# Kernel optimization log

Hardware: AMD Instinct MI355X
Metric: run time of the kernel (lower is better)

The kernel has to match this reference:

```python
import math
import jax, jax.numpy as jnp
import numpy as np

B, T, D = 4, 1024, 1024
H = 16
HD = D // H       # head_dim
DE = 64           # d_event
NT = 8            # n_event_types
NR = 64           # n_rules
NH = 4            # n_hits
NA = 2            # n_alternatives
SQ = math.sqrt(HD)


def setup_inputs() -> dict:
    key = jax.random.key(0)
    ks = jax.random.split(key, 16)
    s = 0.02
    f = jnp.float32
    return {
        "x": jax.random.normal(ks[0], (B, T, D), f),
        "W_node": jax.random.normal(ks[1], (D, D), f) * s,
        "W_value": jax.random.normal(ks[2], (D, D), f) * s,
        "W_out": jax.random.normal(ks[3], (D, D), f) * s,
        "arity_w": jax.random.normal(ks[4], (H, HD), f) * s,   # arity=3 -> one extra axis weight
        "W_event": jax.random.normal(ks[5], (D, DE), f) * s,
        "W_type": jax.random.normal(ks[6], (D, NT), f) * s,
        "patterns": jax.random.normal(ks[7], (NR, DE), f) * s,
        "W_actions": jax.random.normal(ks[8], (NA, D, D), f) * s,
        "W_alt": jax.random.normal(ks[9], (DE, NA), f) * s,
        "log_temp": jnp.zeros((), f),
        "Wg1": jax.random.normal(ks[10], (2 * D + 1, D), f) * s,
        "bg1": jnp.zeros((D,), f),
        "Wg2": jax.random.normal(ks[11], (D, 1), f) * s,
        "bg2": jnp.zeros((1,), f),
    }


def reference(x, W_node, W_value, W_out, arity_w, W_event, W_type, patterns,
              W_actions, W_alt, log_temp, Wg1, bg1, Wg2, bg2):
    # --- IsotropicAttention (arity=3, eval mode so dropout is identity) ---
    nodes = (x @ W_node).reshape(B, T, H, HD).transpose(0, 2, 1, 3)    # (B,H,T,HD)
    values = (x @ W_value).reshape(B, T, H, HD).transpose(0, 2, 1, 3)  # (B,H,T,HD)
    scores = jnp.einsum('bhtd,bhsd->bhts', nodes, nodes)
    scores = (scores + scores.transpose(0, 1, 3, 2)) * (0.5 / SQ)      # symmetrize + scale
    ax = jnp.einsum('bhtd,hd->bht', nodes, arity_w)                    # ternary axis score
    mod = jax.nn.sigmoid((ax[:, :, :, None] + ax[:, :, None, :]) / SQ)
    scores = scores * mod
    attn = jax.nn.softmax(scores, axis=-1)
    attn_out = jnp.einsum('bhts,bhsd->bthd', attn, values).reshape(B, T, D) @ W_out
    x1 = x + attn_out
    # --- EventGenerator ---
    events = x1 @ W_event                                              # (B,T,DE)
    event_types = jax.nn.softmax(x1 @ W_type, axis=-1)                 # (B,T,NT)
    # --- RuleBank: soft top-k hit activation ---
    en = events / jnp.maximum(jnp.linalg.norm(events, axis=-1, keepdims=True), 1e-12)
    pn = patterns / jnp.maximum(jnp.linalg.norm(patterns, axis=-1, keepdims=True), 1e-12)
    sim = en @ pn.T                                                    # (B,T,NR)
    topk_vals, topk_idx = jax.lax.top_k(sim, NH)
    temp = jnp.clip(jnp.exp(log_temp), 0.01, 10.0)
    hit_w = jax.nn.softmax(topk_vals / temp, axis=-1)                  # (B,T,NH)
    hit_patterns = patterns[topk_idx]                                  # (B,T,NH,DE)
    weighted_pattern = jnp.einsum('btkd,btk->btd', hit_patterns, hit_w)
    alt_w = jax.nn.softmax((weighted_pattern @ W_alt) / temp, axis=-1) # (B,T,NA)
    acted = jnp.einsum('btd,ade->btae', x1, W_actions)                 # (B,T,NA,D)
    actions_out = jnp.einsum('btae,bta->bte', acted, alt_w)
    hit_strength = jnp.max(topk_vals, axis=-1, keepdims=True)
    actions_out = actions_out * jax.nn.sigmoid(hit_strength)
    # --- TransactionGate: soft commit/rollback ---
    entropy = -jnp.sum(event_types * jnp.log(event_types + 1e-10), axis=-1, keepdims=True)
    entropy_norm = entropy / math.log(NT)
    gin = jnp.concatenate([x1, actions_out, entropy_norm], axis=-1)    # (B,T,2D+1)
    g = jax.nn.sigmoid(jax.nn.silu(gin @ Wg1 + bg1) @ Wg2 + bg2)       # (B,T,1)
    return x1 + g * actions_out
```

## Files before the change

### kernel.cpp

```cpp
#include <hip/hip_runtime.h>
#include <hip/hip_bf16.h>
#include <math.h>

#define B_  4
#define T_  1024
#define D_  1024
#define H_  16
#define HD_ 64
#define DE_ 64
#define NT_ 8
#define NR_ 64
#define NH_ 4

typedef __attribute__((ext_vector_type(8))) short short8;
typedef __attribute__((ext_vector_type(4))) short short4v;
typedef __attribute__((ext_vector_type(2))) unsigned uint2v;
typedef __attribute__((ext_vector_type(4))) float f4;

__device__ __forceinline__ short f2bf(float f) {
    unsigned x = __float_as_uint(f);
    unsigned r = (x + 0x7fffu + ((x >> 16) & 1u)) >> 16;
    return (short)r;
}
__device__ __forceinline__ float bf2f(short s) {
    return __uint_as_float(((unsigned)(unsigned short)s) << 16);
}

__device__ __forceinline__ int swz64(int row, int slot) {
    return row * 64 + ((slot ^ (row & 7)) << 3);
}

__global__ __launch_bounds__(256) void castx_k(
    const float* __restrict__ x, short* __restrict__ xb)
{
    size_t i = ((size_t)blockIdx.x * 256 + threadIdx.x) * 8;
    float4 v0 = *(const float4*)&x[i];
    float4 v1 = *(const float4*)&x[i + 4];
    short8 o;
    o[0] = f2bf(v0.x); o[1] = f2bf(v0.y); o[2] = f2bf(v0.z); o[3] = f2bf(v0.w);
    o[4] = f2bf(v1.x); o[5] = f2bf(v1.y); o[6] = f2bf(v1.z); o[7] = f2bf(v1.w);
    *(short8*)&xb[i] = o;
}

struct TJ { const float* src; short* dst; int K, N, rs, ro, base; };
struct TJobs { TJ j[7]; };

__global__ __launch_bounds__(256) void tcast_all(TJobs jb)
{
    int bid = blockIdx.x;
    int ji = 0;
#pragma unroll
    for (int i = 1; i < 7; i++) if (bid >= jb.j[i].base) ji = i;
    const float* src = jb.j[ji].src;
    short* dst = jb.j[ji].dst;
    const int K = jb.j[ji].K, N = jb.j[ji].N;
    const int rs = jb.j[ji].rs, ro = jb.j[ji].ro;
    int rel = bid - jb.j[ji].base;
    int tiles_n = N >> 6;
    int k0 = (rel / tiles_n) * 64, n0 = (rel % tiles_n) * 64;

    __shared__ float tile[64][65];
    const int tid = threadIdx.x;
    const int r = tid >> 4, c = (tid & 15) * 4;
#pragma unroll
    for (int rep = 0; rep < 4; rep++) {
        int rr = rep * 16 + r;
        float4 v = *(const float4*)&src[(size_t)(k0 + rr) * N + n0 + c];
        tile[rr][c] = v.x; tile[rr][c + 1] = v.y; tile[rr][c + 2] = v.z; tile[rr][c + 3] = v.w;
    }
    __syncthreads();
#pragma unroll
    for (int rep = 0; rep < 4; rep++) {
        int n = rep * 16 + r;
        short4v p;
        p[0] = f2bf(tile[c + 0][n]);
        p[1] = f2bf(tile[c + 1][n]);
        p[2] = f2bf(tile[c + 2][n]);
        p[3] = f2bf(tile[c + 3][n]);
        *(short4v*)&dst[(size_t)((n0 + n) * rs + ro) * K + k0 + c] = p;
    }
}

__global__ __launch_bounds__(256) void ttype_k(
    const float* __restrict__ Wt, short* __restrict__ BTe)
{
    int idx = blockIdx.x * 256 + threadIdx.x;
    int n = idx >> 10, k = idx & 1023;
    BTe[(size_t)(64 + n) * 1024 + k] = f2bf(Wt[k * 8 + n]);
}

template<int AM>
__global__ __launch_bounds__(256) void gemm8(
    const short* __restrict__ A1, const short* __restrict__ A2, int Ks,
    const short* __restrict__ BT,
    float* __restrict__ C, short* __restrict__ Cb1, short* __restrict__ Cb2,
    int M, int N, int K, int epi,
    const float* __restrict__ resid, const float* __restrict__ ent,
    const float* __restrict__ w1e, const float* __restrict__ bias,
    const float* __restrict__ altw, const float* __restrict__ hitsig)
{
    constexpr int BM = AM * 32;
    constexpr int AR = (AM == 4) ? 2 : 4;
    constexpr int ANV = 64 / AR / 8;
    __shared__ short As[BM * 72];
    __shared__ short Bs[64 * 72];
    const int tid = threadIdx.x, wave = tid >> 6, lane = tid & 63;
    const int lrow = lane & 15, lq = lane >> 4;
    int bid = blockIdx.x;
    int tiles_m = M / BM;
    int mpx = tiles_m >> 3;
    int xcd = bid & 7, idx = bid >> 3;
    int mt = xcd * mpx + (idx % mpx);
    int nt = idx / mpx;
    const int m0 = mt * BM, n0 = nt * 64;
    const int wm = (wave >> 1) * (AM * 16), wn = (wave & 1) * 32;
    const int K2 = K - Ks;
    const int arow = tid / AR, ash = (tid % AR) * (64 / AR);
    const int brow = tid >> 2, bsh = (tid & 3) * 16;

    short8 va[ANV], vb[2];
    auto loadA = [&](int k0) {
        int ka = k0 + ash;
        const short* ap = (ka < Ks)
            ? A1 + (size_t)(m0 + arow) * Ks + ka
            : A2 + (size_t)(m0 + arow) * K2 + (ka - Ks);
#pragma unroll
        for (int u = 0; u < ANV; u++) va[u] = *(const short8*)(ap + u * 8);
    };
    auto loadB = [&](int k0) {
        const short* bp = BT + (size_t)(n0 + brow) * K + k0 + bsh;
#pragma unroll
        for (int u = 0; u < 2; u++) vb[u] = *(const short8*)(bp + u * 8);
    };

    loadA(0); loadB(0);
    f4 acc[AM][2] = {};

    for (int k0 = 0; k0 < K; k0 += 64) {
        __syncthreads();
#pragma unroll
        for (int u = 0; u < ANV; u++)
            *(short8*)&As[arow * 72 + ash + u * 8] = va[u];
#pragma unroll
        for (int u = 0; u < 2; u++)
            *(short8*)&Bs[brow * 72 + bsh + u * 8] = vb[u];
        __syncthreads();
        if (k0 + 64 < K) { loadA(k0 + 64); loadB(k0 + 64); }
        __builtin_amdgcn_sched_barrier(0);
#pragma unroll
        for (int kh = 0; kh < 2; kh++) {
            short8 af[AM], bfv[2];
#pragma unroll
            for (int i = 0; i < AM; i++)
                af[i] = *(short8*)&As[(wm + i * 16 + lrow) * 72 + kh * 32 + lq * 8];
#pragma unroll
            for (int j = 0; j < 2; j++)
                bfv[j] = *(short8*)&Bs[(wn + j * 16 + lrow) * 72 + kh * 32 + lq * 8];
#pragma unroll
            for (int i = 0; i < AM; i++)
#pragma unroll
                for (int j = 0; j < 2; j++)
                    acc[i][j] = __builtin_amdgcn_mfma_f32_16x16x32_bf16(
                        af[i], bfv[j], acc[i][j], 0, 0, 0);
        }
    }

#pragma unroll
    for (int i = 0; i < AM; i++) {
#pragma unroll
        for (int r = 0; r < 4; r++) {
            int row = m0 + wm + i * 16 + lq * 4 + r;
            float w0 = 0.f, w1 = 0.f, hs = 0.f;
            if (epi == 5) { w0 = altw[row * 2]; w1 = altw[row * 2 + 1]; hs = hitsig[row]; }
#pragma unroll
            for (int j = 0; j < 2; j++) {
                int col = n0 + wn + j * 16 + lrow;
                float v = acc[i][j][r];
                if (epi == 0) {
                    C[(size_t)row * N + col] = v;
                } else if (epi == 1) {
                    v += resid[(size_t)row * N + col];
                    C[(size_t)row * N + col] = v;
                    Cb1[(size_t)row * N + col] = f2bf(v);
                } else if (epi == 2) {
                    if (col < 1024) Cb1[(size_t)row * 1024 + col] = f2bf(v);
                    else            Cb2[(size_t)row * 1024 + col - 1024] = f2bf(v);
                } else if (epi == 3) {
                    v += ent[row] * w1e[col] + bias[col];
                    float sv = v * __builtin_amdgcn_rcpf(1.f + __expf(-v));
                    Cb1[(size_t)row * N + col] = f2bf(sv);
                } else {
                    float other = __shfl_xor(v, 1);
                    if ((lane & 1) == 0) {
                        float cv = (w0 * v + w1 * other) * hs;
                        Cb1[(size_t)row * 1024 + (col >> 1)] = f2bf(cv);
                    }
                }
            }
        }
    }
}

__global__ __launch_bounds__(256) void vtrans_k(
    const short* __restrict__ vb, short* __restrict__ vtg)
{
    const int b = blockIdx.z, h = blockIdx.y, t0 = blockIdx.x * 64;
    const int tid = threadIdx.x;
    __shared__ short tile[64 * 72];
    const int row = tid >> 2, c = (tid & 3) * 16;
    const short* p = vb + (size_t)(b * T_ + t0 + row) * D_ + h * 64 + c;
    *(short8*)&tile[row * 72 + c + 0] = *(const short8*)(p + 0);
    *(short8*)&tile[row * 72 + c + 8] = *(const short8*)(p + 8);
    __syncthreads();
    short8 o0, o1;
#pragma unroll
    for (int i = 0; i < 8; i++) o0[i] = tile[(c + i) * 72 + row];
#pragma unroll
    for (int i = 0; i < 8; i++) o1[i] = tile[(c + 8 + i) * 72 + row];
    short* q = vtg + (size_t)((b * H_ + h) * 64 + row) * T_ + t0 + c;
    *(short8*)(q + 0) = o0;
    *(short8*)(q + 8) = o1;
}

__global__ __launch_bounds__(256) void ax_k(
    const short* __restrict__ nodes_bf, const float* __restrict__ arity_w,
    float* __restrict__ ax)
{
    int idx = blockIdx.x * 256 + threadIdx.x;
    int t = idx & (T_ - 1);
    int h = (idx >> 10) & (H_ - 1);
    int b = idx >> 14;
    const short* np_ = nodes_bf + (((size_t)b * T_ + t) * H_ + h) * HD_;
    float s = 0.f;
#pragma unroll
    for (int d = 0; d < HD_; d += 8) {
        short8 n8 = *(const short8*)&np_[d];
#pragma unroll
        for (int q = 0; q < 8; q++) s += bf2f(n8[q]) * arity_w[h * HD_ + d + q];
    }
    ax[idx] = s;
}

__global__ __launch_bounds__(256) void attn9_k(
    const short* __restrict__ nodes_bf, const short* __restrict__ vtg,
    const float* __restrict__ ax, short* __restrict__ attnp)
{
    const int b = blockIdx.z, h = blockIdx.y, t0 = blockIdx.x * 64;
    const int tid = threadIdx.x;
    const int wave = tid >> 6, lane = tid & 63;
    const int lrow = lane & 15, lq = lane >> 4;
    const int wm = wave * 16;
    const int row = tid >> 2, c4 = tid & 3;

    __shared__ short Ns[2][64 * 64];
    __shared__ short Vt[2][64 * 64];
    __shared__ short Pm[64 * 64];

    const short* qp = nodes_bf + (size_t)(b * T_ + t0 + wm + lrow) * D_ + h * 64;
    const short8 bt0 = *(const short8*)(qp + lq * 8);
    const short8 bt1 = *(const short8*)(qp + 32 + lq * 8);
    const float at8 = ax[(size_t)(b * H_ + h) * T_ + t0 + wm + lrow] * 0.125f;

    const short* np0 = nodes_bf + (size_t)(b * T_ + row) * D_ + h * 64 + c4 * 16;
    const short* vp0 = vtg + (size_t)((b * H_ + h) * 64 + row) * T_ + c4 * 16;
    const float* axp_ = ax + (size_t)(b * H_ + h) * T_;

    short8 vn0, vn1, vv0, vv1;
    f4 axv[4];
    auto preload = [&](int s0) {
        const short* np = np0 + (size_t)s0 * D_;
        const short* vp = vp0 + s0;
        vn0 = *(const short8*)(np + 0);
        vn1 = *(const short8*)(np + 8);
        vv0 = *(const short8*)(vp + 0);
        vv1 = *(const short8*)(vp + 8);
#pragma unroll
        for (int j = 0; j < 4; j++)
            axv[j] = *(const f4*)&axp_[s0 + j * 16 + lq * 4];
    };

    preload(0);

    float l_reg = 0.f;
    f4 O[4] = {};
    f4 axc[4];

    for (int t = 0; t < T_ / 64; t++) {
        const int cur = t & 1;
        *(short8*)&Ns[cur][swz64(row, 2 * c4 + 0)] = vn0;
        *(short8*)&Ns[cur][swz64(row, 2 * c4 + 1)] = vn1;
        *(short8*)&Vt[cur][swz64(row, 2 * c4 + 0)] = vv0;
        *(short8*)&Vt[cur][swz64(row, 2 * c4 + 1)] = vv1;
#pragma unroll
        for (int j = 0; j < 4; j++) axc[j] = axv[j];
        __syncthreads();
        if (t + 1 < T_ / 64) preload((t + 1) * 64);
        __builtin_amdgcn_sched_barrier(0);

        float psum = 0.f;
#pragma unroll
        for (int j = 0; j < 4; j++) {
            short8 a0 = *(short8*)&Ns[cur][swz64(j * 16 + lrow, lq)];
            short8 a1 = *(short8*)&Ns[cur][swz64(j * 16 + lrow, 4 + lq)];
            f4 s = {0.f, 0.f, 0.f, 0.f};
            __builtin_amdgcn_s_setprio(1);
            s = __builtin_amdgcn_mfma_f32_16x16x32_bf16(a0, bt0, s, 0, 0, 0);
            s = __builtin_amdgcn_mfma_f32_16x16x32_bf16(a1, bt1, s, 0, 0, 0);
            __builtin_amdgcn_s_setprio(0);
            float p0, p1, p2, p3;
            {
                float z, zz, t1, mK;
                z = fmaf(axc[j][0], 0.125f, at8); zz = z * z;
                t1 = fmaf(zz, -0.0037570183f, 0.04508422f);
                mK = fmaf(z, t1, 0.09016844f);
                p0 = __builtin_amdgcn_exp2f(s[0] * mK);
                z = fmaf(axc[j][1], 0.125f, at8); zz = z * z;
                t1 = fmaf(zz, -0.0037570183f, 0.04508422f);
                mK = fmaf(z, t1, 0.09016844f);
                p1 = __builtin_amdgcn_exp2f(s[1] * mK);
                z = fmaf(axc[j][2], 0.125f, at8); zz = z * z;
                t1 = fmaf(zz, -0.0037570183f, 0.04508422f);
                mK = fmaf(z, t1, 0.09016844f);
                p2 = __builtin_amdgcn_exp2f(s[2] * mK);
                z = fmaf(axc[j][3], 0.125f, at8); zz = z * z;
                t1 = fmaf(zz, -0.0037570183f, 0.04508422f);
                mK = fmaf(z, t1, 0.09016844f);
                p3 = __builtin_amdgcn_exp2f(s[3] * mK);
            }
            psum += (p0 + p1) + (p2 + p3);
            unsigned u0, u1;
            asm("v_cvt_pk_bf16_f32 %0, %1, %2" : "=v"(u0) : "v"(p0), "v"(p1));
            asm("v_cvt_pk_bf16_f32 %0, %1, %2" : "=v"(u1) : "v"(p2), "v"(p3));
            uint2v uu; uu[0] = u0; uu[1] = u1;
            *(uint2v*)&Pm[swz64(wm + lrow, 2 * j + (lq >> 1)) + (lq & 1) * 4] = uu;
        }
        l_reg += psum;

        short8 pa0 = *(short8*)&Pm[swz64(wm + lrow, lq)];
        short8 pa1 = *(short8*)&Pm[swz64(wm + lrow, 4 + lq)];
        __builtin_amdgcn_s_setprio(1);
#pragma unroll
        for (int dj = 0; dj < 4; dj++) {
            short8 v0 = *(short8*)&Vt[cur][swz64(dj * 16 + lrow, lq)];
            short8 v1 = *(short8*)&Vt[cur][swz64(dj * 16 + lrow, 4 + lq)];
            O[dj] = __builtin_amdgcn_mfma_f32_16x16x32_bf16(pa0, v0, O[dj], 0, 0, 0);
            O[dj] = __builtin_amdgcn_mfma_f32_16x16x32_bf16(pa1, v1, O[dj], 0, 0, 0);
        }
        __builtin_amdgcn_s_setprio(0);
    }

    l_reg += __shfl_xor(l_reg, 16);
    l_reg += __shfl_xor(l_reg, 32);

    float linv[4];
#pragma unroll
    for (int r = 0; r < 4; r++)
        linv[r] = __builtin_amdgcn_rcpf(__shfl(l_reg, lq * 4 + r));
#pragma unroll
    for (int dj = 0; dj < 4; dj++)
#pragma unroll
        for (int r = 0; r < 4; r++)
            attnp[(size_t)(b * T_ + t0 + wm + lq * 4 + r) * D_ + h * 64 + dj * 16 + lrow] =
                f2bf(O[dj][r] * linv[r]);
}

__global__ __launch_bounds__(64) void pnorm_k(
    const float* __restrict__ patterns, float* __restrict__ pn)
{
    int r = blockIdx.x, lane = threadIdx.x;
    float v = patterns[r * 64 + lane];
    float ss = v * v;
    for (int off = 1; off < 64; off <<= 1) ss += __shfl_xor(ss, off);
    pn[r * 64 + lane] = v / fmaxf(sqrtf(ss), 1e-12f);
}

__global__ __launch_bounds__(256) void token2_k(
    const float* __restrict__ evlg, const float* __restrict__ pn,
    const float* __restrict__ patterns, const float* __restrict__ W_alt,
    const float* __restrict__ log_temp,
    float* __restrict__ entn, float* __restrict__ altw, float* __restrict__ hitsig)
{
    const int tid = threadIdx.x, wave = tid >> 6, lane = tid & 63;
    __shared__ float pn_sh[64 * 68];
    __shared__ float pat_sh[64 * 68];
    __shared__ float en_sh[4][68];
    {
        int row = tid >> 2, c = (tid & 3) * 16;
#pragma unroll
        for (int u = 0; u < 4; u++) {
            *(float4*)&pn_sh[row * 68 + c + u * 4]  = *(const float4*)&pn[row * 64 + c + u * 4];
            *(float4*)&pat_sh[row * 68 + c + u * 4] = *(const float4*)&patterns[row * 64 + c + u * 4];
        }
    }
    float temp = expf(log_temp[0]);
    temp = fminf(fmaxf(temp, 0.01f), 10.f);
    const float tinv = 1.f / temp;
    __syncthreads();

#pragma unroll
    for (int rep = 0; rep < 2; rep++) {
        const int m = blockIdx.x * 8 + wave * 2 + rep;
        float ev = evlg[(size_t)m * 128 + lane];
        float ss = ev * ev;
        for (int off = 1; off < 64; off <<= 1) ss += __shfl_xor(ss, off);
        float en = ev * __builtin_amdgcn_rcpf(fmaxf(sqrtf(ss), 1e-12f));
        en_sh[wave][lane] = en;
        float entv;
        {
            float lgt = evlg[(size_t)m * 128 + 64 + (lane & 7)];
            float mx = lgt;
            for (int off = 1; off < 8; off <<= 1) mx = fmaxf(mx, __shfl_xor(mx, off));
            float p = __expf(lgt - mx);
            float sum = p;
            for (int off = 1; off < 8; off <<= 1) sum += __shfl_xor(sum, off);
            float pi = p / sum;
            float term = -pi * __logf(pi + 1e-10f);
            float e = term;
            for (int off = 1; off < 8; off <<= 1) e += __shfl_xor(e, off);
            entv = e * 0.4808983f;
        }
        float sim = 0.f;
#pragma unroll
        for (int u = 0; u < 16; u++) {
            float4 e4 = *(float4*)&en_sh[wave][u * 4];
            float4 p4 = *(float4*)&pn_sh[lane * 68 + u * 4];
            sim += e4.x * p4.x + e4.y * p4.y + e4.z * p4.z + e4.w * p4.w;
        }
        float v = sim;
        float tv[NH_]; int tix[NH_];
#pragma unroll
        for (int kk = 0; kk < NH_; kk++) {
            float mv = v; int mi = lane;
            if (v == -1e30f) mi = 127;
            for (int off = 1; off < 64; off <<= 1) {
                float ov = __shfl_xor(mv, off);
                int   oi = __shfl_xor(mi, off);
                if (ov > mv || (ov == mv && oi < mi)) { mv = ov; mi = oi; }
            }
            tv[kk] = mv; tix[kk] = mi;
            if (lane == mi) v = -1e30f;
        }
        float hmx = tv[0];
        float hw[NH_], hsum = 0.f;
#pragma unroll
        for (int kk = 0; kk < NH_; kk++) { hw[kk] = __expf((tv[kk] - hmx) * tinv); hsum += hw[kk]; }
        float hsr = __builtin_amdgcn_rcpf(hsum);
        float wp = 0.f;
#pragma unroll
        for (int kk = 0; kk < NH_; kk++) wp += hw[kk] * hsr * pat_sh[tix[kk] * 68 + lane];
        float a0 = wp * W_alt[lane * 2 + 0];
        float a1 = wp * W_alt[lane * 2 + 1];
        for (int off = 1; off < 64; off <<= 1) {
            a0 += __shfl_xor(a0, off);
            a1 += __shfl_xor(a1, off);
        }
        a0 *= tinv; a1 *= tinv;
        float amx = fmaxf(a0, a1);
        float e0 = __expf(a0 - amx), e1 = __expf(a1 - amx);
        if (lane == 0) {
            float zr = __builtin_amdgcn_rcpf(e0 + e1);
            altw[m * 2 + 0] = e0 * zr;
            altw[m * 2 + 1] = e1 * zr;
            hitsig[m] = __builtin_amdgcn_rcpf(1.f + __expf(-tv[0]));
            entn[m] = entv;
        }
    }
}

__global__ __launch_bounds__(256) void gate_k(
    const short* __restrict__ h1_bf, const float* __restrict__ Wg2,
    const float* __restrict__ bg2, const float* __restrict__ x1,
    const short* __restrict__ actions_bf, float* __restrict__ out)
{
    const int m = blockIdx.x, tid = threadIdx.x;
    float part = 0.f;
    for (int d = tid; d < D_; d += 256)
        part += bf2f(h1_bf[(size_t)m * D_ + d]) * Wg2[d];
    __shared__ float red[256];
    red[tid] = part;
    __syncthreads();
    for (int w = 128; w > 0; w >>= 1) {
        if (tid < w) red[tid] += red[tid + w];
        __syncthreads();
    }
    float g = 1.f / (1.f + expf(-(red[0] + bg2[0])));
    for (int d = tid; d < D_; d += 256) {
        size_t i = (size_t)m * D_ + d;
        out[i] = x1[i] + g * bf2f(actions_bf[i]);
    }
}

extern "C" void kernel_launch(void* const* d_in, const int* in_sizes, int n_in,
                              void* d_out, int out_size, void* d_ws, size_t ws_size,
                              hipStream_t stream)
{
    const float* x        = (const float*)d_in[0];
    const float* W_node   = (const float*)d_in[1];
    const float* W_value  = (const float*)d_in[2];
    const float* W_out    = (const float*)d_in[3];
    const float* arity_w  = (const float*)d_in[4];
    const float* W_event  = (const float*)d_in[5];
    const float* W_type   = (const float*)d_in[6];
    const float* patterns = (const float*)d_in[7];
    const float* W_act    = (const float*)d_in[8];
    const float* W_alt    = (const float*)d_in[9];
    const float* log_temp = (const float*)d_in[10];
    const float* Wg1      = (const float*)d_in[11];
    const float* bg1      = (const float*)d_in[12];
    const float* Wg2      = (const float*)d_in[13];
    const float* bg2      = (const float*)d_in[14];
    float* out = (float*)d_out;

    const int M = B_ * T_;
    float* x1     = (float*)d_ws;
    float* evlg   = x1 + 4194304;
    float* axp    = evlg + 524288;
    float* pn     = axp + 65536;
    float* entn   = pn + 4096;
    float* altw   = entn + 4096;
    float* hitsig = altw + 8192;
    short* big       = (short*)(hitsig + 4096);
    short* xbf       = big;
    short* nodes_bf  = big + 1 * 4194304;
    short* values_bf = big + 2 * 4194304;
    short* vtg       = big + 3 * 4194304;
    short* x1_bf     = big + 4 * 4194304;
    short* wts       = big + 5 * 4194304;
    short* WnvT  = wts;
    short* WoT   = wts + 2 * 1048576;
    short* WaT   = wts + 3 * 1048576;
    short* Wg1T  = wts + 5 * 1048576;
    short* BTe   = wts + 7 * 1048576;
    short* actions_bf = vtg;
    short* h1_bf      = xbf;

    dim3 blk(256);
    dim3 g_bh(T_ / 64, H_, B_);

    castx_k<<<2048, blk, 0, stream>>>(x, xbf);
    pnorm_k<<<NR_, 64, 0, stream>>>(patterns, pn);
    TJobs jb;
    jb.j[0] = {W_node,            WnvT,           1024, 1024, 1, 0,    0};
    jb.j[1] = {W_value,           WnvT + 1048576, 1024, 1024, 1, 0,  256};
    jb.j[2] = {W_out,             WoT,            1024, 1024, 1, 0,  512};
    jb.j[3] = {W_act,             WaT,            1024, 1024, 2, 0,  768};
    jb.j[4] = {W_act + 1048576,   WaT,            1024, 1024, 2, 1, 1024};
    jb.j[5] = {Wg1,               Wg1T,           2048, 1024, 1, 0, 1280};
    jb.j[6] = {W_event,           BTe,            1024,   64, 1, 0, 1792};
    tcast_all<<<1808, blk, 0, stream>>>(jb);
    ttype_k<<<32, blk, 0, stream>>>(W_type, BTe);

    gemm8<4><<<1024, blk, 0, stream>>>(xbf, xbf, D_, WnvT,
        nullptr, nodes_bf, values_bf, M, 2048, D_, 2,
        nullptr, nullptr, nullptr, nullptr, nullptr, nullptr);
    ax_k<<<256, blk, 0, stream>>>(nodes_bf, arity_w, axp);
    vtrans_k<<<g_bh, blk, 0, stream>>>(values_bf, vtg);
    attn9_k<<<g_bh, blk, 0, stream>>>(nodes_bf, vtg, axp, xbf);
    gemm8<2><<<1024, blk, 0, stream>>>(xbf, xbf, D_, WoT,
        x1, x1_bf, nullptr, M, D_, D_, 1,
        x, nullptr, nullptr, nullptr, nullptr, nullptr);
    gemm8<2><<<128, blk, 0, stream>>>(x1_bf, x1_bf, D_, BTe,
        evlg, nullptr, nullptr, M, 128, D_, 0,
        nullptr, nullptr, nullptr, nullptr, nullptr, nullptr);
    token2_k<<<M / 8, blk, 0, stream>>>(evlg, pn, patterns, W_alt, log_temp,
                                        entn, altw, hitsig);
    gemm8<4><<<1024, blk, 0, stream>>>(x1_bf, x1_bf, D_, WaT,
        nullptr, actions_bf, nullptr, M, 2048, D_, 5,
        nullptr, nullptr, nullptr, nullptr, altw, hitsig);
    gemm8<2><<<1024, blk, 0, stream>>>(x1_bf, actions_bf, D_, Wg1T,
        nullptr, h1_bf, nullptr, M, D_, 2048, 3,
        nullptr, entn, Wg1 + (size_t)2048 * D_, bg1, nullptr, nullptr);
    gate_k<<<M, blk, 0, stream>>>(h1_bf, Wg2, bg2, x1, actions_bf, out);
}
```

Baseline: 321.4 us.

## Fuse gate dot product into GEMM epilogue and merge small prep kernels

```diff
diff --git a/kernel.cpp b/kernel.cpp
--- a/kernel.cpp
+++ b/kernel.cpp
@@ -30,63 +30,73 @@
     return row * 64 + ((slot ^ (row & 7)) << 3);
 }
 
-__global__ __launch_bounds__(256) void castx_k(
-    const float* __restrict__ x, short* __restrict__ xb)
-{
-    size_t i = ((size_t)blockIdx.x * 256 + threadIdx.x) * 8;
-    float4 v0 = *(const float4*)&x[i];
-    float4 v1 = *(const float4*)&x[i + 4];
-    short8 o;
-    o[0] = f2bf(v0.x); o[1] = f2bf(v0.y); o[2] = f2bf(v0.z); o[3] = f2bf(v0.w);
-    o[4] = f2bf(v1.x); o[5] = f2bf(v1.y); o[6] = f2bf(v1.z); o[7] = f2bf(v1.w);
-    *(short8*)&xb[i] = o;
-}
-
 struct TJ { const float* src; short* dst; int K, N, rs, ro, base; };
 struct TJobs { TJ j[7]; };
 
-__global__ __launch_bounds__(256) void tcast_all(TJobs jb)
-{
-    int bid = blockIdx.x;
-    int ji = 0;
-#pragma unroll
-    for (int i = 1; i < 7; i++) if (bid >= jb.j[i].base) ji = i;
-    const float* src = jb.j[ji].src;
-    short* dst = jb.j[ji].dst;
-    const int K = jb.j[ji].K, N = jb.j[ji].N;
-    const int rs = jb.j[ji].rs, ro = jb.j[ji].ro;
-    int rel = bid - jb.j[ji].base;
-    int tiles_n = N >> 6;
-    int k0 = (rel / tiles_n) * 64, n0 = (rel % tiles_n) * 64;
-
+__global__ __launch_bounds__(256) void prep_k(
+    const float* __restrict__ x, short* __restrict__ xb, TJobs jb,
+    const float* __restrict__ Wt, short* __restrict__ BTe,
+    const float* __restrict__ patterns, float* __restrict__ pn)
+{
+    const int bid = blockIdx.x;
+    const int tid = threadIdx.x;
     __shared__ float tile[64][65];
-    const int tid = threadIdx.x;
-    const int r = tid >> 4, c = (tid & 15) * 4;
-#pragma unroll
-    for (int rep = 0; rep < 4; rep++) {
-        int rr = rep * 16 + r;
-        float4 v = *(const float4*)&src[(size_t)(k0 + rr) * N + n0 + c];
-        tile[rr][c] = v.x; tile[rr][c + 1] = v.y; tile[rr][c + 2] = v.z; tile[rr][c + 3] = v.w;
-    }
-    __syncthreads();
-#pragma unroll
-    for (int rep = 0; rep < 4; rep++) {
-        int n = rep * 16 + r;
-        short4v p;
-        p[0] = f2bf(tile[c + 0][n]);
-        p[1] = f2bf(tile[c + 1][n]);
-        p[2] = f2bf(tile[c + 2][n]);
-        p[3] = f2bf(tile[c + 3][n]);
-        *(short4v*)&dst[(size_t)((n0 + n) * rs + ro) * K + k0 + c] = p;
-    }
-}
-
-__global__ __launch_bounds__(256) void ttype_k(
-    const float* __restrict__ Wt, short* __restrict__ BTe)
-{
-    int idx = blockIdx.x * 256 + threadIdx.x;
-    int n = idx >> 10, k = idx & 1023;
-    BTe[(size_t)(64 + n) * 1024 + k] = f2bf(Wt[k * 8 + n]);
+
+    if (bid < 2048) {
+        size_t i = ((size_t)bid * 256 + tid) * 8;
+        float4 v0 = *(const float4*)&x[i];
+        float4 v1 = *(const float4*)&x[i + 4];
+        short8 o;
+        o[0] = f2bf(v0.x); o[1] = f2bf(v0.y); o[2] = f2bf(v0.z); o[3] = f2bf(v0.w);
+        o[4] = f2bf(v1.x); o[5] = f2bf(v1.y); o[6] = f2bf(v1.z); o[7] = f2bf(v1.w);
+        *(short8*)&xb[i] = o;
+        return;
+    }
+    if (bid < 3856) {
+        int ji = 0;
+#pragma unroll
+        for (int i = 1; i < 7; i++) if (bid >= jb.j[i].base) ji = i;
+        const float* src = jb.j[ji].src;
+        short* dst = jb.j[ji].dst;
+        const int K = jb.j[ji].K, N = jb.j[ji].N;
+        const int rs = jb.j[ji].rs, ro = jb.j[ji].ro;
+        int rel = bid - jb.j[ji].base;
+        int tiles_n = N >> 6;
+        int k0 = (rel / tiles_n) * 64, n0 = (rel % tiles_n) * 64;
+        const int r = tid >> 4, c = (tid & 15) * 4;
+#pragma unroll
+        for (int rep = 0; rep < 4; rep++) {
+            int rr = rep * 16 + r;
+            float4 v = *(const float4*)&src[(size_t)(k0 + rr) * N + n0 + c];
+            tile[rr][c] = v.x; tile[rr][c + 1] = v.y; tile[rr][c + 2] = v.z; tile[rr][c + 3] = v.w;
+        }
+        __syncthreads();
+#pragma unroll
+        for (int rep = 0; rep < 4; rep++) {
+            int n = rep * 16 + r;
+            short4v p;
+            p[0] = f2bf(tile[c + 0][n]);
+            p[1] = f2bf(tile[c + 1][n]);
+            p[2] = f2bf(tile[c + 2][n]);
+            p[3] = f2bf(tile[c + 3][n]);
+            *(short4v*)&dst[(size_t)((n0 + n) * rs + ro) * K + k0 + c] = p;
+        }
+        return;
+    }
+    if (bid < 3888) {
+        int idx = (bid - 3856) * 256 + tid;
+        int n = idx >> 10, k = idx & 1023;
+        BTe[(size_t)(64 + n) * 1024 + k] = f2bf(Wt[k * 8 + n]);
+        return;
+    }
+    {
+        int r = (bid - 3888) * 4 + (tid >> 6);
+        int lane = tid & 63;
+        float v = patterns[r * 64 + lane];
+        float ss = v * v;
+        for (int off = 1; off < 64; off <<= 1) ss += __shfl_xor(ss, off);
+        pn[r * 64 + lane] = v / fmaxf(sqrtf(ss), 1e-12f);
+    }
 }
 
 template<int AM>
@@ -165,6 +175,30 @@
         }
     }
 
+    if (epi == 3) {
+#pragma unroll
+        for (int i = 0; i < AM; i++) {
+#pragma unroll
+            for (int r = 0; r < 4; r++) {
+                int row = m0 + wm + i * 16 + lq * 4 + r;
+                float gp = 0.f;
+#pragma unroll
+                for (int j = 0; j < 2; j++) {
+                    int col = n0 + wn + j * 16 + lrow;
+                    float v = acc[i][j][r] + ent[row] * w1e[col] + bias[col];
+                    float sv = v * __builtin_amdgcn_rcpf(1.f + __expf(-v));
+                    gp += sv * altw[col];
+                }
+                gp += __shfl_xor(gp, 1);
+                gp += __shfl_xor(gp, 2);
+                gp += __shfl_xor(gp, 4);
+                gp += __shfl_xor(gp, 8);
+                if (lrow == 0) atomicAdd(&C[row], gp);
+            }
+        }
+        return;
+    }
+
 #pragma unroll
     for (int i = 0; i < AM; i++) {
 #pragma unroll
@@ -185,10 +219,6 @@
                 } else if (epi == 2) {
                     if (col < 1024) Cb1[(size_t)row * 1024 + col] = f2bf(v);
                     else            Cb2[(size_t)row * 1024 + col - 1024] = f2bf(v);
-                } else if (epi == 3) {
-                    v += ent[row] * w1e[col] + bias[col];
-                    float sv = v * __builtin_amdgcn_rcpf(1.f + __expf(-v));
-                    Cb1[(size_t)row * N + col] = f2bf(sv);
                 } else {
                     float other = __shfl_xor(v, 1);
                     if ((lane & 1) == 0) {
@@ -201,44 +231,47 @@
     }
 }
 
-__global__ __launch_bounds__(256) void vtrans_k(
-    const short* __restrict__ vb, short* __restrict__ vtg)
-{
-    const int b = blockIdx.z, h = blockIdx.y, t0 = blockIdx.x * 64;
+__global__ __launch_bounds__(256) void vx_k(
+    const short* __restrict__ vb, short* __restrict__ vtg,
+    const short* __restrict__ nodes_bf, const float* __restrict__ arity_w,
+    float* __restrict__ ax)
+{
+    const int bid = blockIdx.x;
     const int tid = threadIdx.x;
     __shared__ short tile[64 * 72];
-    const int row = tid >> 2, c = (tid & 3) * 16;
-    const short* p = vb + (size_t)(b * T_ + t0 + row) * D_ + h * 64 + c;
-    *(short8*)&tile[row * 72 + c + 0] = *(const short8*)(p + 0);
-    *(short8*)&tile[row * 72 + c + 8] = *(const short8*)(p + 8);
-    __syncthreads();
-    short8 o0, o1;
-#pragma unroll
-    for (int i = 0; i < 8; i++) o0[i] = tile[(c + i) * 72 + row];
-#pragma unroll
-    for (int i = 0; i < 8; i++) o1[i] = tile[(c + 8 + i) * 72 + row];
-    short* q = vtg + (size_t)((b * H_ + h) * 64 + row) * T_ + t0 + c;
-    *(short8*)(q + 0) = o0;
-    *(short8*)(q + 8) = o1;
-}
-
-__global__ __launch_bounds__(256) void ax_k(
-    const short* __restrict__ nodes_bf, const float* __restrict__ arity_w,
-    float* __restrict__ ax)
-{
-    int idx = blockIdx.x * 256 + threadIdx.x;
-    int t = idx & (T_ - 1);
-    int h = (idx >> 10) & (H_ - 1);
-    int b = idx >> 14;
-    const short* np_ = nodes_bf + (((size_t)b * T_ + t) * H_ + h) * HD_;
-    float s = 0.f;
-#pragma unroll
-    for (int d = 0; d < HD_; d += 8) {
-        short8 n8 = *(const short8*)&np_[d];
-#pragma unroll
-        for (int q = 0; q < 8; q++) s += bf2f(n8[q]) * arity_w[h * HD_ + d + q];
-    }
-    ax[idx] = s;
+
+    if (bid < 1024) {
+        const int b = bid >> 8, h = (bid >> 4) & 15, t0 = (bid & 15) * 64;
+        const int row = tid >> 2, c = (tid & 3) * 16;
+        const short* p = vb + (size_t)(b * T_ + t0 + row) * D_ + h * 64 + c;
+        *(short8*)&tile[row * 72 + c + 0] = *(const short8*)(p + 0);
+        *(short8*)&tile[row * 72 + c + 8] = *(const short8*)(p + 8);
+        __syncthreads();
+        short8 o0, o1;
+#pragma unroll
+        for (int i = 0; i < 8; i++) o0[i] = tile[(c + i) * 72 + row];
+#pragma unroll
+        for (int i = 0; i < 8; i++) o1[i] = tile[(c + 8 + i) * 72 + row];
+        short* q = vtg + (size_t)((b * H_ + h) * 64 + row) * T_ + t0 + c;
+        *(short8*)(q + 0) = o0;
+        *(short8*)(q + 8) = o1;
+        return;
+    }
+    {
+        int idx = (bid - 1024) * 256 + tid;
+        int t = idx & (T_ - 1);
+        int h = (idx >> 10) & (H_ - 1);
+        int b = idx >> 14;
+        const short* np_ = nodes_bf + (((size_t)b * T_ + t) * H_ + h) * HD_;
+        float s = 0.f;
+#pragma unroll
+        for (int d = 0; d < HD_; d += 8) {
+            short8 n8 = *(const short8*)&np_[d];
+#pragma unroll
+            for (int q = 0; q < 8; q++) s += bf2f(n8[q]) * arity_w[h * HD_ + d + q];
+        }
+        ax[idx] = s;
+    }
 }
 
 __global__ __launch_bounds__(256) void attn9_k(
@@ -364,21 +397,12 @@
                 f2bf(O[dj][r] * linv[r]);
 }
 
-__global__ __launch_bounds__(64) void pnorm_k(
-    const float* __restrict__ patterns, float* __restrict__ pn)
-{
-    int r = blockIdx.x, lane = threadIdx.x;
-    float v = patterns[r * 64 + lane];
-    float ss = v * v;
-    for (int off = 1; off < 64; off <<= 1) ss += __shfl_xor(ss, off);
-    pn[r * 64 + lane] = v / fmaxf(sqrtf(ss), 1e-12f);
-}
-
 __global__ __launch_bounds__(256) void token2_k(
     const float* __restrict__ evlg, const float* __restrict__ pn,
     const float* __restrict__ patterns, const float* __restrict__ W_alt,
     const float* __restrict__ log_temp,
-    float* __restrict__ entn, float* __restrict__ altw, float* __restrict__ hitsig)
+    float* __restrict__ entn, float* __restrict__ altw, float* __restrict__ hitsig,
+    float* __restrict__ gsum)
 {
     const int tid = threadIdx.x, wave = tid >> 6, lane = tid & 63;
     __shared__ float pn_sh[64 * 68];
@@ -463,31 +487,27 @@
             altw[m * 2 + 1] = e1 * zr;
             hitsig[m] = __builtin_amdgcn_rcpf(1.f + __expf(-tv[0]));
             entn[m] = entv;
-        }
-    }
-}
-
-__global__ __launch_bounds__(256) void gate_k(
-    const short* __restrict__ h1_bf, const float* __restrict__ Wg2,
-    const float* __restrict__ bg2, const float* __restrict__ x1,
-    const short* __restrict__ actions_bf, float* __restrict__ out)
+            gsum[m] = 0.f;
+        }
+    }
+}
+
+__global__ __launch_bounds__(256) void gate2_k(
+    const float* __restrict__ gsum, const float* __restrict__ bg2,
+    const float* __restrict__ x1, const short* __restrict__ actions_bf,
+    float* __restrict__ out)
 {
     const int m = blockIdx.x, tid = threadIdx.x;
-    float part = 0.f;
-    for (int d = tid; d < D_; d += 256)
-        part += bf2f(h1_bf[(size_t)m * D_ + d]) * Wg2[d];
-    __shared__ float red[256];
-    red[tid] = part;
-    __syncthreads();
-    for (int w = 128; w > 0; w >>= 1) {
-        if (tid < w) red[tid] += red[tid + w];
-        __syncthreads();
-    }
-    float g = 1.f / (1.f + expf(-(red[0] + bg2[0])));
-    for (int d = tid; d < D_; d += 256) {
-        size_t i = (size_t)m * D_ + d;
-        out[i] = x1[i] + g * bf2f(actions_bf[i]);
-    }
+    float g = 1.f / (1.f + __expf(-(gsum[m] + bg2[0])));
+    size_t i = (size_t)m * D_ + tid * 4;
+    float4 xv = *(const float4*)&x1[i];
+    short4v av = *(const short4v*)&actions_bf[i];
+    float4 o;
+    o.x = xv.x + g * bf2f(av[0]);
+    o.y = xv.y + g * bf2f(av[1]);
+    o.z = xv.z + g * bf2f(av[2]);
+    o.w = xv.w + g * bf2f(av[3]);
+    *(float4*)&out[i] = o;
 }
 
 extern "C" void kernel_launch(void* const* d_in, const int* in_sizes, int n_in,
@@ -519,6 +539,7 @@
     float* entn   = pn + 4096;
     float* altw   = entn + 4096;
     float* hitsig = altw + 8192;
+    float* gsum   = axp;
     short* big       = (short*)(hitsig + 4096);
     short* xbf       = big;
     short* nodes_bf  = big + 1 * 4194304;
@@ -532,29 +553,24 @@
     short* Wg1T  = wts + 5 * 1048576;
     short* BTe   = wts + 7 * 1048576;
     short* actions_bf = vtg;
-    short* h1_bf      = xbf;
 
     dim3 blk(256);
     dim3 g_bh(T_ / 64, H_, B_);
 
-    castx_k<<<2048, blk, 0, stream>>>(x, xbf);
-    pnorm_k<<<NR_, 64, 0, stream>>>(patterns, pn);
     TJobs jb;
-    jb.j[0] = {W_node,            WnvT,           1024, 1024, 1, 0,    0};
-    jb.j[1] = {W_value,           WnvT + 1048576, 1024, 1024, 1, 0,  256};
-    jb.j[2] = {W_out,             WoT,            1024, 1024, 1, 0,  512};
-    jb.j[3] = {W_act,             WaT,            1024, 1024, 2, 0,  768};
-    jb.j[4] = {W_act + 1048576,   WaT,            1024, 1024, 2, 1, 1024};
-    jb.j[5] = {Wg1,               Wg1T,           2048, 1024, 1, 0, 1280};
-    jb.j[6] = {W_event,           BTe,            1024,   64, 1, 0, 1792};
-    tcast_all<<<1808, blk, 0, stream>>>(jb);
-    ttype_k<<<32, blk, 0, stream>>>(W_type, BTe);
+    jb.j[0] = {W_node,            WnvT,           1024, 1024, 1, 0, 2048};
+    jb.j[1] = {W_value,           WnvT + 1048576, 1024, 1024, 1, 0, 2304};
+    jb.j[2] = {W_out,             WoT,            1024, 1024, 1, 0, 2560};
+    jb.j[3] = {W_act,             WaT,            1024, 1024, 2, 0, 2816};
+    jb.j[4] = {W_act + 1048576,   WaT,            1024, 1024, 2, 1, 3072};
+    jb.j[5] = {Wg1,               Wg1T,           2048, 1024, 1, 0, 3328};
+    jb.j[6] = {W_event,           BTe,            1024,   64, 1, 0, 3840};
+    prep_k<<<3904, blk, 0, stream>>>(x, xbf, jb, W_type, BTe, patterns, pn);
 
     gemm8<4><<<1024, blk, 0, stream>>>(xbf, xbf, D_, WnvT,
         nullptr, nodes_bf, values_bf, M, 2048, D_, 2,
         nullptr, nullptr, nullptr, nullptr, nullptr, nullptr);
-    ax_k<<<256, blk, 0, stream>>>(nodes_bf, arity_w, axp);
-    vtrans_k<<<g_bh, blk, 0, stream>>>(values_bf, vtg);
+    vx_k<<<1280, blk, 0, stream>>>(values_bf, vtg, nodes_bf, arity_w, axp);
     attn9_k<<<g_bh, blk, 0, stream>>>(nodes_bf, vtg, axp, xbf);
     gemm8<2><<<1024, blk, 0, stream>>>(xbf, xbf, D_, WoT,
         x1, x1_bf, nullptr, M, D_, D_, 1,
@@ -563,12 +579,12 @@
         evlg, nullptr, nullptr, M, 128, D_, 0,
         nullptr, nullptr, nullptr, nullptr, nullptr, nullptr);
     token2_k<<<M / 8, blk, 0, stream>>>(evlg, pn, patterns, W_alt, log_temp,
-                                        entn, altw, hitsig);
+                                        entn, altw, hitsig, gsum);
     gemm8<4><<<1024, blk, 0, stream>>>(x1_bf, x1_bf, D_, WaT,
         nullptr, actions_bf, nullptr, M, 2048, D_, 5,
         nullptr, nullptr, nullptr, nullptr, altw, hitsig);
     gemm8<2><<<1024, blk, 0, stream>>>(x1_bf, actions_bf, D_, Wg1T,
-        nullptr, h1_bf, nullptr, M, D_, 2048, 3,
-        nullptr, entn, Wg1 + (size_t)2048 * D_, bg1, nullptr, nullptr);
-    gate_k<<<M, blk, 0, stream>>>(h1_bf, Wg2, bg2, x1, actions_bf, out);
-}
+        gsum, nullptr, nullptr, M, D_, 2048, 3,
+        nullptr, entn, Wg1 + (size_t)2048 * D_, bg1, Wg2, nullptr);
+    gate2_k<<<M, blk, 0, stream>>>(gsum, bg2, x1, actions_bf, out);
+}
```

Result: no change. 315.6 us, median of 2 (-1.8%).
